# Performance work log

Measured on AMD Instinct MI355X. Metric: run time of the kernel, lower is better.

The kernel has to match this reference:

```python
import jax, jax.numpy as jnp
import numpy as np
from jax import lax

DIM = 384
D_STATE = 16
EXPAND = 2
D_INNER = DIM * EXPAND
B, H, W = 8, 32, 32


def setup_inputs() -> dict:
    key = jax.random.key(0)
    ks = jax.random.split(key, 16)
    s = 0.02
    return {
        'x': jax.random.normal(ks[0], (B, H, W, DIM), jnp.float32),
        'ln_g': jnp.ones((DIM,), jnp.float32),
        'ln_b': jnp.zeros((DIM,), jnp.float32),
        'mlp_w1': jax.random.normal(ks[1], (4, 32), jnp.float32) * s,
        'mlp_b1': jnp.zeros((32,), jnp.float32),
        'mlp_w2': jax.random.normal(ks[2], (32, 4), jnp.float32) * s,
        'mlp_b2': jnp.zeros((4,), jnp.float32),
        'in_proj_w': jax.random.normal(ks[3], (DIM, 2 * D_INNER), jnp.float32) * s,
        'conv_w': jax.random.normal(ks[4], (D_INNER, 1, 3), jnp.float32) * s,
        'conv_b': jnp.zeros((D_INNER,), jnp.float32),
        'x_proj_w': jax.random.normal(ks[5], (D_INNER, 2 * D_STATE), jnp.float32) * s,
        'dt_w': jax.random.normal(ks[6], (D_INNER, D_INNER), jnp.float32) * s,
        'dt_b': jnp.zeros((D_INNER,), jnp.float32),
        'A_log': jax.random.normal(ks[7], (D_INNER, D_STATE), jnp.float32) * 0.01,
        'D': jnp.ones((D_INNER,), jnp.float32),
        'out_proj_w': jax.random.normal(ks[8], (D_INNER, DIM), jnp.float32) * s,
    }


def _select_direction(xn, mlp_w1, mlp_b1, mlp_w2, mlp_b2):
    # GradientDirectionSelector (topk=1 -> argmax)
    b, h, w, _ = xn.shape
    xg = xn.mean(-1)[:, None]                                   # [B,1,H,W]
    xp = jnp.pad(xg, ((0, 0), (0, 0), (1, 1), (1, 1)), mode='reflect')
    kh = jnp.array([-1.0, 0.0, 1.0], xn.dtype).reshape(1, 1, 1, 3)
    kv = jnp.array([-1.0, 0.0, 1.0], xn.dtype).reshape(1, 1, 3, 1)
    dn = ('NCHW', 'OIHW', 'NCHW')
    gh = jnp.abs(lax.conv_general_dilated(xp, kh, (1, 1), 'VALID', dimension_numbers=dn))  # [B,1,H+2,W]
    gv = jnp.abs(lax.conv_general_dilated(xp, kv, (1, 1), 'VALID', dimension_numbers=dn))  # [B,1,H,W+2]
    gh = jax.image.resize(gh, (b, 1, h, w), 'bilinear')
    gv = jax.image.resize(gv, (b, 1, h, w), 'bilinear')
    gd = (gh + gv) * 0.5
    ga = jnp.abs(gh - gv)

    def pool_mean(g):  # avg_pool2d(3, stride=1, pad=1, count_include_pad=True), then spatial mean
        p = lax.reduce_window(g, 0.0, lax.add, (1, 1, 3, 3), (1, 1, 1, 1),
                              [(0, 0), (0, 0), (1, 1), (1, 1)]) / 9.0
        return p.mean(axis=(2, 3))  # [B,1]

    scores = jnp.concatenate([pool_mean(gh), pool_mean(gv), pool_mean(gd), pool_mean(ga)], axis=1)
    logits = jax.nn.relu(scores @ mlp_w1 + mlp_b1) @ mlp_w2 + mlp_b2
    return jnp.argmax(logits, axis=-1)  # softmax is monotone; topk(1) == argmax


def _ssm(seq, in_proj_w, conv_w, conv_b, x_proj_w, dt_w, dt_b, A_log, D, out_proj_w):
    b, L, _ = seq.shape
    xz = seq @ in_proj_w
    xc, z = xz[..., :D_INNER], xz[..., D_INNER:]
    xcc = jnp.swapaxes(xc, 1, 2)  # [B,Di,L]
    xcc = lax.conv_general_dilated(xcc, conv_w, (1,), [(1, 1)],
                                   feature_group_count=D_INNER,
                                   dimension_numbers=('NCH', 'OIH', 'NCH')) + conv_b[None, :, None]
    xc = jax.nn.silu(jnp.swapaxes(xcc, 1, 2))  # [B,L,Di]
    BC = xc @ x_proj_w
    Bm, Cm = BC[..., :D_STATE], BC[..., D_STATE:]
    delta = jax.nn.softplus(xc @ dt_w + dt_b)
    A = -jnp.exp(A_log)
    dA = jnp.exp(jnp.einsum('bld,dn->bldn', delta, A))        # [B,L,Di,N]
    dBx = (delta * xc)[..., None] * Bm[:, :, None, :]          # [B,L,Di,N]

    def step(hst, inp):
        dA_t, dBx_t, C_t = inp
        hst = dA_t * hst + dBx_t
        return hst, jnp.einsum('bdn,bn->bd', hst, C_t)

    h0 = jnp.zeros((b, D_INNER, D_STATE), xc.dtype)
    _, ys = lax.scan(step, h0, (jnp.swapaxes(dA, 0, 1), jnp.swapaxes(dBx, 0, 1), jnp.swapaxes(Cm, 0, 1)))
    y = jnp.swapaxes(ys, 0, 1) + D * xc
    y = y * jax.nn.silu(z)
    return y @ out_proj_w


def reference(x, ln_g, ln_b, mlp_w1, mlp_b1, mlp_w2, mlp_b2,
              in_proj_w, conv_w, conv_b, x_proj_w, dt_w, dt_b, A_log, D, out_proj_w):
    b, h, w, c = x.shape
    mu = x.mean(-1, keepdims=True)
    var = jnp.mean((x - mu) ** 2, axis=-1, keepdims=True)
    xn = (x - mu) / jnp.sqrt(var + 1e-5) * ln_g + ln_b

    idx = _select_direction(xn, mlp_w1, mlp_b1, mlp_w2, mlp_b2)  # [B]
    # DIRECTIONS_4: only 'vertical' (idx 1) changes scan order (transpose H/W);
    # diag directions alias horizontal in the source. Unscan is always (h w).
    is_vert = (idx % 4 == 1)[:, None, None, None]
    x_in = jnp.where(is_vert, jnp.swapaxes(xn, 1, 2), xn)  # requires H == W
    seq = x_in.reshape(b, h * w, c)
    out = _ssm(seq, in_proj_w, conv_w, conv_b, x_proj_w, dt_w, dt_b, A_log, D, out_proj_w)
    return x + out.reshape(b, h, w, c)
```

## Files before the change

kernel.cpp:

```cpp
#include <hip/hip_runtime.h>
#include <hip/hip_bf16.h>
#include <math.h>

#define NPOS 8192
#define DIMC 384
#define DIN 768
#define DST 16
#define CHUNK 16
#define NCH 64

typedef unsigned int uint;
typedef __attribute__((ext_vector_type(8))) short bf16x8;
typedef __attribute__((ext_vector_type(4))) float f32x4;

__device__ __forceinline__ float b2f(unsigned short u) {
    return __uint_as_float(((unsigned int)u) << 16);
}
__device__ __forceinline__ uint cvt_pk(float lo, float hi) {
    uint r;
    asm("v_cvt_pk_bf16_f32 %0, %1, %2" : "=v"(r) : "v"(lo), "v"(hi));
    return r;
}
__device__ __forceinline__ unsigned short f2b1(float f) {
    return (unsigned short)cvt_pk(f, f);
}
__device__ __forceinline__ float frcp(float x) {
    float r;
    asm("v_rcp_f32 %0, %1" : "=v"(r) : "v"(x));
    return r;
}
__device__ __forceinline__ float fexp2(float x) {
    float r;
    asm("v_exp_f32 %0, %1" : "=v"(r) : "v"(x));
    return r;
}
__device__ __forceinline__ void ub8(uint4 u, float* o) {
    o[0] = b2f((unsigned short)(u.x & 0xffff));
    o[1] = b2f((unsigned short)(u.x >> 16));
    o[2] = b2f((unsigned short)(u.y & 0xffff));
    o[3] = b2f((unsigned short)(u.y >> 16));
    o[4] = b2f((unsigned short)(u.z & 0xffff));
    o[5] = b2f((unsigned short)(u.z >> 16));
    o[6] = b2f((unsigned short)(u.w & 0xffff));
    o[7] = b2f((unsigned short)(u.w >> 16));
}
__device__ __forceinline__ void ld_bf8(const unsigned short* p, float* o) {
    ub8(*(const uint4*)p, o);
}
__device__ __forceinline__ uint4 pack_bf8(const float* o) {
    uint4 p;
    p.x = cvt_pk(o[0], o[1]);
    p.y = cvt_pk(o[2], o[3]);
    p.z = cvt_pk(o[4], o[5]);
    p.w = cvt_pk(o[6], o[7]);
    return p;
}
#define LOG2E 1.442695040888963f

__global__ __launch_bounds__(256) void k_ln(const float* __restrict__ x,
        const float* __restrict__ g, const float* __restrict__ bta,
        unsigned short* __restrict__ xnb, float* __restrict__ xg) {
    int wid = blockIdx.x * 4 + (threadIdx.x >> 6);
    int lane = threadIdx.x & 63;
    const float* xr = x + (size_t)wid * DIMC;
    float v[6];
    float s = 0.f, ss = 0.f;
#pragma unroll
    for (int i = 0; i < 6; i++) {
        v[i] = xr[lane + i * 64];
        s += v[i]; ss += v[i] * v[i];
    }
#pragma unroll
    for (int m = 32; m; m >>= 1) { s += __shfl_xor(s, m); ss += __shfl_xor(ss, m); }
    float mu = s * (1.f / DIMC);
    float var = ss * (1.f / DIMC) - mu * mu;
    float rstd = rsqrtf(var + 1e-5f);
    unsigned short* xnr = xnb + (size_t)wid * DIMC;
    float sn = 0.f;
#pragma unroll
    for (int i = 0; i < 6; i++) {
        int c = lane + i * 64;
        float o = (v[i] - mu) * rstd * g[c] + bta[c];
        xnr[c] = f2b1(o);
        sn += o;
    }
#pragma unroll
    for (int m = 32; m; m >>= 1) sn += __shfl_xor(sn, m);
    if (lane == 0) xg[wid] = sn * (1.f / DIMC);
}

__global__ __launch_bounds__(256) void k_dir(const float* __restrict__ xg,
        const float* __restrict__ w1, const float* __restrict__ b1,
        const float* __restrict__ w2, const float* __restrict__ b2,
        int* __restrict__ vert) {
    __shared__ float sg[32][32];
    __shared__ float red[4][4];
    int b = blockIdx.x;
    int tid = threadIdx.x;
    for (int i = tid; i < 1024; i += 256) sg[i >> 5][i & 31] = xg[b * 1024 + i];
    __syncthreads();
    float ph = 0, pv = 0, pd = 0, pa = 0;
    const float iks = 1.f / 1.0625f;
    for (int p = tid; p < 1024; p += 256) {
        int y = p >> 5, xq = p & 31;
        int xl = (xq >= 1) ? xq - 1 : 1;
        int xr2 = (xq <= 30) ? xq + 1 : 30;
        float sf = (y + 0.5f) * 1.0625f - 0.5f;
        int jlo = (int)ceilf(sf - 1.0625f); if (jlo < 0) jlo = 0;
        int jhi = (int)floorf(sf + 1.0625f); if (jhi > 33) jhi = 33;
        float acc = 0.f, wsum = 0.f;
        for (int j = jlo; j <= jhi; j++) {
            float wgt = 1.f - fabsf(sf - j) * iks;
            if (wgt <= 0.f) continue;
            int ry = (j >= 1) ? ((j <= 32) ? j - 1 : 30) : 1;
            acc += wgt * fabsf(sg[ry][xr2] - sg[ry][xl]);
            wsum += wgt;
        }
        float ghr = acc / wsum;
        int yu = (y >= 1) ? y - 1 : 1;
        int yd = (y <= 30) ? y + 1 : 30;
        float sfx = (xq + 0.5f) * 1.0625f - 0.5f;
        int ilo = (int)ceilf(sfx - 1.0625f); if (ilo < 0) ilo = 0;
        int ihi = (int)floorf(sfx + 1.0625f); if (ihi > 33) ihi = 33;
        float accv = 0.f, wsv = 0.f;
        for (int i = ilo; i <= ihi; i++) {
            float wgt = 1.f - fabsf(sfx - i) * iks;
            if (wgt <= 0.f) continue;
            int rx = (i >= 1) ? ((i <= 32) ? i - 1 : 30) : 1;
            accv += wgt * fabsf(sg[yd][rx] - sg[yu][rx]);
            wsv += wgt;
        }
        float gvr = accv / wsv;
        float gd = (ghr + gvr) * 0.5f;
        float ga = fabsf(ghr - gvr);
        float cw = ((y == 0 || y == 31) ? 2.f : 3.f) * ((xq == 0 || xq == 31) ? 2.f : 3.f);
        ph += ghr * cw; pv += gvr * cw; pd += gd * cw; pa += ga * cw;
    }
#pragma unroll
    for (int m = 32; m; m >>= 1) {
        ph += __shfl_xor(ph, m); pv += __shfl_xor(pv, m);
        pd += __shfl_xor(pd, m); pa += __shfl_xor(pa, m);
    }
    int wv = tid >> 6;
    if ((tid & 63) == 0) { red[wv][0] = ph; red[wv][1] = pv; red[wv][2] = pd; red[wv][3] = pa; }
    __syncthreads();
    if (tid == 0) {
        float sc[4];
        for (int k = 0; k < 4; k++)
            sc[k] = (red[0][k] + red[1][k] + red[2][k] + red[3][k]) * (1.f / 9216.f);
        float hdn[32];
        for (int j = 0; j < 32; j++) {
            float a = b1[j];
            for (int i = 0; i < 4; i++) a += sc[i] * w1[i * 32 + j];
            hdn[j] = a > 0.f ? a : 0.f;
        }
        float best = -1e30f; int bi = 0;
        for (int k = 0; k < 4; k++) {
            float a = b2[k];
            for (int j = 0; j < 32; j++) a += hdn[j] * w2[j * 4 + k];
            if (a > best) { best = a; bi = k; }
        }
        vert[b] = (bi == 1) ? 1 : 0;
    }
}

__device__ __forceinline__ void wt_body(const float* __restrict__ W,
        unsigned short* __restrict__ WT, int K, int N, int bid, int tid,
        float (*t)[33]) {
    int nb = N >> 5;
    int n0 = (bid % nb) << 5, k0 = (bid / nb) << 5;
    int kr = tid >> 3, n4 = (tid & 7) << 2;
    float4 v = *(const float4*)(W + (size_t)(k0 + kr) * N + n0 + n4);
    t[kr][n4 + 0] = v.x; t[kr][n4 + 1] = v.y; t[kr][n4 + 2] = v.z; t[kr][n4 + 3] = v.w;
    __syncthreads();
    int nr = tid >> 3, k4 = (tid & 7) << 2;
    ushort4 o;
    o.x = f2b1(t[k4 + 0][nr]); o.y = f2b1(t[k4 + 1][nr]);
    o.z = f2b1(t[k4 + 2][nr]); o.w = f2b1(t[k4 + 3][nr]);
    *(ushort4*)(WT + (size_t)(n0 + nr) * K + k0 + k4) = o;
}

__global__ __launch_bounds__(256) void k_prep(const float* __restrict__ inw,
        const float* __restrict__ dtw, const float* __restrict__ xpw,
        const float* __restrict__ outw,
        unsigned short* __restrict__ inwT, unsigned short* __restrict__ dtwTp,
        unsigned short* __restrict__ outwT) {
    __shared__ float t[32][33];
    int bid = blockIdx.x;
    int tid = threadIdx.x;
    if (bid < 576) {
        wt_body(inw, inwT, 384, 1536, bid, tid, t);
    } else if (bid < 1152) {
        wt_body(dtw, dtwTp, 768, 768, bid - 576, tid, t);
    } else if (bid < 1176) {
        wt_body(xpw, dtwTp + 768 * 768, 768, 32, bid - 1152, tid, t);
    } else if (bid < 1464) {
        wt_body(outw, outwT, 768, 384, bid - 1176, tid, t);
    } else {
        int i = (bid - 1464) * 256 + tid;
        if (i < (96 * 768) / 4)
            *(ushort4*)(dtwTp + 800 * 768 + i * 4) = (ushort4){0, 0, 0, 0};
    }
}

template <int MODE>
__global__ __launch_bounds__(256) void k_mfma(
        const unsigned short* __restrict__ op1,
        const unsigned short* __restrict__ op2,
        void* __restrict__ outp,
        const float* __restrict__ bias,
        const float* __restrict__ resid,
        const int* __restrict__ vert) {
    constexpr int K = (MODE == 0) ? 384 : 768;
    constexpr int NK = K / 32;
    constexpr int NBN = (MODE == 0) ? 12 : (MODE == 1 ? 7 : 3);
    __shared__ unsigned short lds[2][2][128 * 40];
    int tid = threadIdx.x;
    int bid = blockIdx.x;
    int xcd = bid & 7;
    int ii = bid >> 3;
    int n0 = (ii % NBN) << 7;
    int m0 = ((xcd << 3) + ii / NBN) << 7;
    int drow = tid >> 1, dkh = (tid & 1) << 4;

    size_t g1row, g2row;
    if constexpr (MODE == 0) {
        g1row = (size_t)(n0 + drow) * 384;
        int m = m0 + drow;
        int b = m >> 10, l = m & 1023;
        int src = vert[b] ? (((l & 31) << 5) | (l >> 5)) : l;
        g2row = ((size_t)(b << 10) + src) * 384;
    } else if constexpr (MODE == 1) {
        g1row = (size_t)(n0 + drow) * 768;
        g2row = (size_t)(m0 + drow) * 768;
    } else {
        g1row = (size_t)(m0 + drow) * 768;
        g2row = (size_t)(n0 + drow) * 768;
    }

    f32x4 acc[4][4];
    f32x4 zero = {0.f, 0.f, 0.f, 0.f};
#pragma unroll
    for (int i = 0; i < 4; i++)
#pragma unroll
        for (int j = 0; j < 4; j++) acc[i][j] = zero;

    uint4 s1a, s1b, s2a, s2b;
#define LOADS(k0_)                                              \
    { const unsigned short* p1 = op1 + g1row + (k0_) + dkh;     \
      s1a = *(const uint4*)p1; s1b = *(const uint4*)(p1 + 8);   \
      const unsigned short* p2 = op2 + g2row + (k0_) + dkh;     \
      s2a = *(const uint4*)p2; s2b = *(const uint4*)(p2 + 8); }
#define WRITES(buf_)                                            \
    { *(uint4*)&lds[buf_][0][drow * 40 + dkh] = s1a;            \
      *(uint4*)&lds[buf_][0][drow * 40 + dkh + 8] = s1b;        \
      *(uint4*)&lds[buf_][1][drow * 40 + dkh] = s2a;            \
      *(uint4*)&lds[buf_][1][drow * 40 + dkh + 8] = s2b; }

    int wid = tid >> 6, lane = tid & 63;
    int lr = lane & 15, lg = lane >> 4;
    int o1b = (wid >> 1) << 6;
    int o2b = (wid & 1) << 6;

    LOADS(0)
    WRITES(0)
    int cur = 0;
    for (int ks = 0; ks < NK; ks++) {
        int kn = (ks + 1) << 5;
        if (ks + 1 < NK) { LOADS(kn) }
        __syncthreads();
        const unsigned short* L1 = &lds[cur][0][0];
        const unsigned short* L2 = &lds[cur][1][0];
        bf16x8 f1[4], f2[4];
#pragma unroll
        for (int f = 0; f < 4; f++) f1[f] = *(const bf16x8*)&L1[(o1b + f * 16 + lr) * 40 + (lg << 3)];
#pragma unroll
        for (int f = 0; f < 4; f++) f2[f] = *(const bf16x8*)&L2[(o2b + f * 16 + lr) * 40 + (lg << 3)];
#pragma unroll
        for (int i = 0; i < 4; i++)
#pragma unroll
            for (int j = 0; j < 4; j++)
                acc[i][j] = __builtin_amdgcn_mfma_f32_16x16x32_bf16(f1[i], f2[j], acc[i][j], 0, 0, 0);
        if (ks + 1 < NK) { WRITES(cur ^ 1) }
        cur ^= 1;
    }

    if constexpr (MODE <= 1) {
        if (MODE == 1 && n0 == 768) {
            if ((wid >> 1) == 0) {
                float* BCT_ = (float*)resid;
#pragma unroll
                for (int i = 0; i < 2; i++) {
                    int col = i * 16 + lg * 4;
#pragma unroll
                    for (int j = 0; j < 4; j++) {
                        int mb_ = m0 + o2b + j * 16 + lr;
                        float4 v4;
                        v4.x = acc[i][j][0]; v4.y = acc[i][j][1];
                        v4.z = acc[i][j][2]; v4.w = acc[i][j][3];
                        *(float4*)(BCT_ + (size_t)mb_ * 32 + col) = v4;
                    }
                }
            }
        } else {
            __syncthreads();
            unsigned short* lt = &lds[0][0][0];
#pragma unroll
            for (int i = 0; i < 4; i++) {
                int nr = o1b + i * 16 + lg * 4;
#pragma unroll
                for (int j = 0; j < 4; j++) {
                    int mc = o2b + j * 16 + lr;
#pragma unroll
                    for (int r = 0; r < 4; r++) {
                        float v = acc[i][j][r];
                        if constexpr (MODE == 1) {
                            v += bias[n0 + nr + r];
                            v = fmaxf(v, 0.f) + __logf(1.f + __expf(-fabsf(v)));
                        }
                        lt[(nr + r) * 132 + mc] = f2b1(v);
                    }
                }
            }
            __syncthreads();
            unsigned short* CT = (unsigned short*)outp;
#pragma unroll
            for (int ps = 0; ps < 8; ps++) {
                int row = ps * 16 + (tid >> 4);
                uint4 v = *(const uint4*)&lt[row * 132 + (tid & 15) * 8];
                *(uint4*)(CT + (size_t)(n0 + row) * 8192 + m0 + (tid & 15) * 8) = v;
            }
        }
    } else {
        float* C = (float*)outp;
#pragma unroll
        for (int i = 0; i < 4; i++) {
            int mb_ = m0 + o1b + i * 16 + lg * 4;
#pragma unroll
            for (int j = 0; j < 4; j++) {
                int n = n0 + o2b + j * 16 + lr;
#pragma unroll
                for (int r = 0; r < 4; r++) {
                    int m = mb_ + r;
                    C[(size_t)m * 384 + n] = acc[i][j][r] + resid[(size_t)m * 384 + n];
                }
            }
        }
    }
#undef LOADS
#undef WRITES
}

__global__ __launch_bounds__(256) void k_conv(const unsigned short* __restrict__ xzb,
        const float* __restrict__ cw, const float* __restrict__ cb,
        unsigned short* __restrict__ xcT, unsigned short* __restrict__ xcR) {
    __shared__ unsigned short ly[128][64];
    int blk = blockIdx.x;
    int dg = blk % 12, mg = blk / 12;
    int r0 = mg * 128;
    int tid = threadIdx.x;
    int dl = tid >> 2, tq = tid & 3;
    int d = dg * 64 + dl;
    int t0 = r0 + tq * 32;
    const unsigned short* xr = xzb + (size_t)d * 8192;
    float xx[32];
#pragma unroll
    for (int q = 0; q < 4; q++) ub8(*(const uint4*)(xr + t0 + q * 8), xx + q * 8);
    int l0 = t0 & 1023;
    float xprev = (l0 != 0)   ? b2f(xr[t0 - 1])  : 0.f;
    float xnext = (l0 != 992) ? b2f(xr[t0 + 32]) : 0.f;
    float w0 = cw[d * 3], w1 = cw[d * 3 + 1], w2 = cw[d * 3 + 2], bb = cb[d];
    float o[32];
#pragma unroll
    for (int j = 0; j < 32; j++) {
        float v = bb + w1 * xx[j];
        v += w0 * ((j == 0) ? xprev : xx[j - 1]);
        v += w2 * ((j == 31) ? xnext : xx[j + 1]);
        o[j] = v * frcp(1.f + __expf(-v));
    }
    unsigned short* dstT = xcT + (size_t)d * 8192 + t0;
#pragma unroll
    for (int q = 0; q < 4; q++) *(uint4*)(dstT + q * 8) = pack_bf8(o + q * 8);
#pragma unroll
    for (int j = 0; j < 32; j++) ly[tq * 32 + j][dl] = f2b1(o[j]);
    __syncthreads();
#pragma unroll
    for (int k = 0; k < 4; k++) {
        int i = tid + k * 256;
        int row = i >> 3, sg = i & 7;
        uint4 v = *(const uint4*)&ly[row][sg * 8];
        *(uint4*)(xcR + (size_t)(r0 + row) * 768 + dg * 64 + sg * 8) = v;
    }
}

__global__ __launch_bounds__(256) void k_scan1(const unsigned short* __restrict__ xzb,
        const unsigned short* __restrict__ xcT, const float* __restrict__ BCT,
        const float* __restrict__ A_log,
        unsigned short* __restrict__ G, float* __restrict__ sumd) {
    int tid = threadIdx.x;
    int lane = tid & 63;
    int blk = blockIdx.x;
    int dg = blk % 12;
    int cg = (blk / 12) % 16;
    int b  = blk / 192;
    int c = cg * 4 + (tid >> 6);
    int d = dg * 64 + lane;
    int r0i = __builtin_amdgcn_readfirstlane(b * 1024 + c * CHUNK);
    const float* Bu = BCT + (size_t)r0i * 32;
    float Avl[16];
#pragma unroll
    for (int q = 0; q < 4; q++) {
        float4 a4 = *(const float4*)(A_log + d * 16 + q * 4);
        Avl[q * 4 + 0] = -__expf(a4.x) * LOG2E;
        Avl[q * 4 + 1] = -__expf(a4.y) * LOG2E;
        Avl[q * 4 + 2] = -__expf(a4.z) * LOG2E;
        Avl[q * 4 + 3] = -__expf(a4.w) * LOG2E;
    }
    const unsigned short* dptr = xzb + (size_t)d * 8192 + r0i;
    const unsigned short* xptr = xcT + (size_t)d * 8192 + r0i;
    uint4 du[2], xu[2];
#pragma unroll
    for (int q = 0; q < 2; q++) {
        du[q] = *(const uint4*)(dptr + q * 8);
        xu[q] = *(const uint4*)(xptr + q * 8);
    }
    float h[16] = {};
    float sd = 0.f;
#pragma unroll
    for (int q = 0; q < 2; q++) {
        float dv[8], xv[8];
        ub8(du[q], dv);
        ub8(xu[q], xv);
#pragma unroll
        for (int j = 0; j < 8; j++) {
            int t = q * 8 + j;
            float dx = dv[j] * xv[j];
            sd += dv[j];
            float Bt[16];
            *(float4*)&Bt[0]  = *(const float4*)(Bu + t * 32);
            *(float4*)&Bt[4]  = *(const float4*)(Bu + t * 32 + 4);
            *(float4*)&Bt[8]  = *(const float4*)(Bu + t * 32 + 8);
            *(float4*)&Bt[12] = *(const float4*)(Bu + t * 32 + 12);
#pragma unroll
            for (int n = 0; n < 16; n++)
                h[n] = fmaf(fexp2(dv[j] * Avl[n]), h[n], dx * Bt[n]);
        }
    }
    unsigned short* gp = G + (((size_t)(b * NCH + c)) * 768 + d) * 16;
    *(uint4*)gp       = pack_bf8(h);
    *(uint4*)(gp + 8) = pack_bf8(h + 8);
    sumd[(size_t)(b * NCH + c) * 768 + d] = sd;
}

__global__ __launch_bounds__(256) void k_scan2(unsigned short* __restrict__ G,
        const float* __restrict__ sumd, const float* __restrict__ A_log) {
    int blk = blockIdx.x;
    int dg = blk % 48, b = blk / 48;
    int tid = threadIdx.x;
    int dl = tid >> 4, n = tid & 15;
    int d = dg * 16 + dl;
    float Av = -__expf(A_log[d * 16 + n]);
    float H = 0.f;
#pragma unroll 8
    for (int c = 0; c < NCH; c++) {
        size_t gi = (((size_t)(b * NCH + c)) * 768 + d) * 16 + n;
        float Gv = b2f(G[gi]);
        float P = __expf(Av * sumd[(size_t)(b * NCH + c) * 768 + d]);
        G[gi] = f2b1(H);
        H = fmaf(P, H, Gv);
    }
}

__global__ __launch_bounds__(256) void k_scan3(const unsigned short* __restrict__ xzb,
        const unsigned short* __restrict__ xcT, const float* __restrict__ BCT,
        const float* __restrict__ A_log, const float* __restrict__ Dp,
        const unsigned short* __restrict__ G, unsigned short* __restrict__ yR) {
    __shared__ unsigned short ly[64][64];
    int tid = threadIdx.x;
    int lane = tid & 63;
    int wv = tid >> 6;
    int blk = blockIdx.x;
    int dg = blk % 12;
    int cg = (blk / 12) % 16;
    int b  = blk / 192;
    int c = cg * 4 + wv;
    int d = dg * 64 + lane;
    int r0i = __builtin_amdgcn_readfirstlane(b * 1024 + c * CHUNK);
    const float* Bu = BCT + (size_t)r0i * 32;
    float Avl[16];
#pragma unroll
    for (int q = 0; q < 4; q++) {
        float4 a4 = *(const float4*)(A_log + d * 16 + q * 4);
        Avl[q * 4 + 0] = -__expf(a4.x) * LOG2E;
        Avl[q * 4 + 1] = -__expf(a4.y) * LOG2E;
        Avl[q * 4 + 2] = -__expf(a4.z) * LOG2E;
        Avl[q * 4 + 3] = -__expf(a4.w) * LOG2E;
    }
    float Dv = Dp[d];
    const unsigned short* dptr = xzb + (size_t)d * 8192 + r0i;
    const unsigned short* zptr = xzb + (size_t)(768 + d) * 8192 + r0i;
    const unsigned short* xptr = xcT + (size_t)d * 8192 + r0i;
    uint4 du[2], xu[2], zu[2];
#pragma unroll
    for (int q = 0; q < 2; q++) {
        du[q] = *(const uint4*)(dptr + q * 8);
        xu[q] = *(const uint4*)(xptr + q * 8);
        zu[q] = *(const uint4*)(zptr + q * 8);
    }
    float h[16];
    {
        const unsigned short* gp = G + (((size_t)(b * NCH + c)) * 768 + d) * 16;
        ld_bf8(gp, h);
        ld_bf8(gp + 8, h + 8);
    }
#pragma unroll
    for (int q = 0; q < 2; q++) {
        float dv[8], xv[8], zv[8];
        ub8(du[q], dv);
        ub8(xu[q], xv);
        ub8(zu[q], zv);
#pragma unroll
        for (int j = 0; j < 8; j++) {
            int t = q * 8 + j;
            float dx = dv[j] * xv[j];
            float Bt[16], Ct[16];
            *(float4*)&Bt[0]  = *(const float4*)(Bu + t * 32);
            *(float4*)&Bt[4]  = *(const float4*)(Bu + t * 32 + 4);
            *(float4*)&Bt[8]  = *(const float4*)(Bu + t * 32 + 8);
            *(float4*)&Bt[12] = *(const float4*)(Bu + t * 32 + 12);
            *(float4*)&Ct[0]  = *(const float4*)(Bu + t * 32 + 16);
            *(float4*)&Ct[4]  = *(const float4*)(Bu + t * 32 + 20);
            *(float4*)&Ct[8]  = *(const float4*)(Bu + t * 32 + 24);
            *(float4*)&Ct[12] = *(const float4*)(Bu + t * 32 + 28);
            float p0 = 0.f, p1 = 0.f, p2 = 0.f, p3 = 0.f;
#pragma unroll
            for (int n = 0; n < 16; n += 4) {
                h[n + 0] = fmaf(fexp2(dv[j] * Avl[n + 0]), h[n + 0], dx * Bt[n + 0]);
                h[n + 1] = fmaf(fexp2(dv[j] * Avl[n + 1]), h[n + 1], dx * Bt[n + 1]);
                h[n + 2] = fmaf(fexp2(dv[j] * Avl[n + 2]), h[n + 2], dx * Bt[n + 2]);
                h[n + 3] = fmaf(fexp2(dv[j] * Avl[n + 3]), h[n + 3], dx * Bt[n + 3]);
                p0 = fmaf(h[n + 0], Ct[n + 0], p0);
                p1 = fmaf(h[n + 1], Ct[n + 1], p1);
                p2 = fmaf(h[n + 2], Ct[n + 2], p2);
                p3 = fmaf(h[n + 3], Ct[n + 3], p3);
            }
            float p = (p0 + p1) + (p2 + p3);
            float zz = zv[j];
            float sig = frcp(1.f + __expf(-zz));
            ly[wv * 16 + t][lane] = f2b1(fmaf(Dv, xv[j], p) * zz * sig);
        }
    }
    __syncthreads();
    size_t rb = (size_t)b * 1024 + (size_t)cg * 64;
#pragma unroll
    for (int k = 0; k < 2; k++) {
        int i = tid + k * 256;
        int row = i >> 3, sg = i & 7;
        uint4 v = *(const uint4*)&ly[row][sg * 8];
        *(uint4*)(yR + (size_t)(rb + row) * 768 + dg * 64 + sg * 8) = v;
    }
}

extern "C" void kernel_launch(void* const* d_in, const int* in_sizes, int n_in,
                              void* d_out, int out_size, void* d_ws, size_t ws_size,
                              hipStream_t stream) {
    const float* x    = (const float*)d_in[0];
    const float* ln_g = (const float*)d_in[1];
    const float* ln_b = (const float*)d_in[2];
    const float* mw1  = (const float*)d_in[3];
    const float* mb1  = (const float*)d_in[4];
    const float* mw2  = (const float*)d_in[5];
    const float* mb2  = (const float*)d_in[6];
    const float* inw  = (const float*)d_in[7];
    const float* cw   = (const float*)d_in[8];
    const float* cb   = (const float*)d_in[9];
    const float* xpw  = (const float*)d_in[10];
    const float* dtw  = (const float*)d_in[11];
    const float* dtb  = (const float*)d_in[12];
    const float* alog = (const float*)d_in[13];
    const float* Dp   = (const float*)d_in[14];
    const float* outw = (const float*)d_in[15];
    float* out = (float*)d_out;

    char* ws = (char*)d_ws;
    unsigned short* xzb = (unsigned short*)(ws);
    float* BCT = (float*)(ws + 25165824);
    float* xg  = (float*)(ws + 26214400);
    int*  vert = (int*)(ws + 26247168);
    unsigned short* G = (unsigned short*)(ws + 26248192);
    float* sumd = (float*)(ws + 38831104);
    unsigned short* inwT  = (unsigned short*)(ws + 40403968);
    unsigned short* dtwTp = (unsigned short*)(ws + 41583616);
    unsigned short* outwT = (unsigned short*)(ws + 42959872);
    unsigned short* xcR   = (unsigned short*)(ws + 43549696);
    unsigned short* yR    = (unsigned short*)(ws + 56132608);

    unsigned short* xnb = (unsigned short*)d_out;
    unsigned short* xcT = (unsigned short*)d_out;

    k_ln<<<2048, 256, 0, stream>>>(x, ln_g, ln_b, xnb, xg);
    k_dir<<<8, 256, 0, stream>>>(xg, mw1, mb1, mw2, mb2, vert);
    k_prep<<<1536, 256, 0, stream>>>(inw, dtw, xpw, outw, inwT, dtwTp, outwT);
    k_mfma<0><<<12 * 64, 256, 0, stream>>>(inwT, xnb, xzb, nullptr, nullptr, vert);
    k_conv<<<12 * 64, 256, 0, stream>>>(xzb, cw, cb, xcT, xcR);
    k_mfma<1><<<7 * 64, 256, 0, stream>>>(dtwTp, xcR, xzb, dtb, (const float*)BCT, nullptr);
    k_scan1<<<1536, 256, 0, stream>>>(xzb, xcT, BCT, alog, G, sumd);
    k_scan2<<<8 * 48, 256, 0, stream>>>(G, sumd, alog);
    k_scan3<<<1536, 256, 0, stream>>>(xzb, xcT, BCT, alog, Dp, G, yR);
    k_mfma<2><<<3 * 64, 256, 0, stream>>>(yR, outwT, out, nullptr, x, nullptr);
}
```

Baseline: 153.3 us.

## Use 64x128 GEMM tiles with 192-wide K phases loaded in bulk into LDS

```diff
diff --git a/kernel.cpp b/kernel.cpp
--- a/kernel.cpp
+++ b/kernel.cpp
@@ -211,90 +211,104 @@
         const float* __restrict__ bias,
         const float* __restrict__ resid,
         const int* __restrict__ vert) {
-    constexpr int K = (MODE == 0) ? 384 : 768;
-    constexpr int NK = K / 32;
-    constexpr int NBN = (MODE == 0) ? 12 : (MODE == 1 ? 7 : 3);
-    __shared__ unsigned short lds[2][2][128 * 40];
+    constexpr int ldK = (MODE == 0) ? 384 : 768;
+    constexpr int NPH = (MODE == 0) ? 2 : 4;
+    __shared__ unsigned short s1[64 * 200];
+    __shared__ unsigned short s2[128 * 200];
     int tid = threadIdx.x;
     int bid = blockIdx.x;
     int xcd = bid & 7;
     int ii = bid >> 3;
-    int n0 = (ii % NBN) << 7;
-    int m0 = ((xcd << 3) + ii / NBN) << 7;
-    int drow = tid >> 1, dkh = (tid & 1) << 4;
-
-    size_t g1row, g2row;
-    if constexpr (MODE == 0) {
-        g1row = (size_t)(n0 + drow) * 384;
-        int m = m0 + drow;
-        int b = m >> 10, l = m & 1023;
-        int src = vert[b] ? (((l & 31) << 5) | (l >> 5)) : l;
-        g2row = ((size_t)(b << 10) + src) * 384;
-    } else if constexpr (MODE == 1) {
-        g1row = (size_t)(n0 + drow) * 768;
-        g2row = (size_t)(m0 + drow) * 768;
-    } else {
-        g1row = (size_t)(m0 + drow) * 768;
-        g2row = (size_t)(n0 + drow) * 768;
-    }
-
-    f32x4 acc[4][4];
+    int p1, p2;
+    if constexpr (MODE == 0)      { p1 = (ii % 24) << 6; p2 = ((xcd << 3) + ii / 24) << 7; }
+    else if constexpr (MODE == 1) { p1 = (ii % 14) << 6; p2 = ((xcd << 3) + ii / 14) << 7; }
+    else                          { p2 = (ii % 3) << 7;  p1 = ((xcd << 4) + ii / 3) << 6; }
+
+    int vt = 0;
+    if constexpr (MODE == 0) vt = vert[p2 >> 10];
+
+    f32x4 acc[2][4];
     f32x4 zero = {0.f, 0.f, 0.f, 0.f};
 #pragma unroll
-    for (int i = 0; i < 4; i++)
+    for (int i = 0; i < 2; i++)
 #pragma unroll
         for (int j = 0; j < 4; j++) acc[i][j] = zero;
 
-    uint4 s1a, s1b, s2a, s2b;
-#define LOADS(k0_)                                              \
-    { const unsigned short* p1 = op1 + g1row + (k0_) + dkh;     \
-      s1a = *(const uint4*)p1; s1b = *(const uint4*)(p1 + 8);   \
-      const unsigned short* p2 = op2 + g2row + (k0_) + dkh;     \
-      s2a = *(const uint4*)p2; s2b = *(const uint4*)(p2 + 8); }
-#define WRITES(buf_)                                            \
-    { *(uint4*)&lds[buf_][0][drow * 40 + dkh] = s1a;            \
-      *(uint4*)&lds[buf_][0][drow * 40 + dkh + 8] = s1b;        \
-      *(uint4*)&lds[buf_][1][drow * 40 + dkh] = s2a;            \
-      *(uint4*)&lds[buf_][1][drow * 40 + dkh + 8] = s2b; }
-
-    int wid = tid >> 6, lane = tid & 63;
+    int w = tid >> 6, lane = tid & 63;
     int lr = lane & 15, lg = lane >> 4;
-    int o1b = (wid >> 1) << 6;
-    int o2b = (wid & 1) << 6;
-
-    LOADS(0)
-    WRITES(0)
-    int cur = 0;
-    for (int ks = 0; ks < NK; ks++) {
-        int kn = (ks + 1) << 5;
-        if (ks + 1 < NK) { LOADS(kn) }
+    int o1b = (w & 1) << 5;
+    int o2b = (w >> 1) << 6;
+
+    for (int ph = 0; ph < NPH; ph++) {
+        if (ph) __syncthreads();
+        int kc = ph * 192;
+        {
+            uint4 v[6];
+#pragma unroll
+            for (int q = 0; q < 6; q++) {
+                int u = tid + q * 256;
+                int r = u / 24, cb = (u % 24) << 3;
+                v[q] = *(const uint4*)(op1 + (size_t)(p1 + r) * ldK + kc + cb);
+            }
+#pragma unroll
+            for (int q = 0; q < 6; q++) {
+                int u = tid + q * 256;
+                int r = u / 24, cb = (u % 24) << 3;
+                *(uint4*)&s1[r * 200 + cb] = v[q];
+            }
+        }
+#pragma unroll
+        for (int g = 0; g < 2; g++) {
+            uint4 v[6];
+#pragma unroll
+            for (int q = 0; q < 6; q++) {
+                int u = tid + (g * 6 + q) * 256;
+                int r = u / 24, cb = (u % 24) << 3;
+                size_t grow;
+                if constexpr (MODE == 0) {
+                    int m = p2 + r;
+                    int l = m & 1023;
+                    int src = vt ? (((l & 31) << 5) | (l >> 5)) : l;
+                    grow = (size_t)((m & ~1023) + src) * 384;
+                } else {
+                    grow = (size_t)(p2 + r) * 768;
+                }
+                v[q] = *(const uint4*)(op2 + grow + kc + cb);
+            }
+#pragma unroll
+            for (int q = 0; q < 6; q++) {
+                int u = tid + (g * 6 + q) * 256;
+                int r = u / 24, cb = (u % 24) << 3;
+                *(uint4*)&s2[r * 200 + cb] = v[q];
+            }
+        }
         __syncthreads();
-        const unsigned short* L1 = &lds[cur][0][0];
-        const unsigned short* L2 = &lds[cur][1][0];
-        bf16x8 f1[4], f2[4];
-#pragma unroll
-        for (int f = 0; f < 4; f++) f1[f] = *(const bf16x8*)&L1[(o1b + f * 16 + lr) * 40 + (lg << 3)];
-#pragma unroll
-        for (int f = 0; f < 4; f++) f2[f] = *(const bf16x8*)&L2[(o2b + f * 16 + lr) * 40 + (lg << 3)];
-#pragma unroll
-        for (int i = 0; i < 4; i++)
-#pragma unroll
-            for (int j = 0; j < 4; j++)
-                acc[i][j] = __builtin_amdgcn_mfma_f32_16x16x32_bf16(f1[i], f2[j], acc[i][j], 0, 0, 0);
-        if (ks + 1 < NK) { WRITES(cur ^ 1) }
-        cur ^= 1;
+#pragma unroll
+        for (int st = 0; st < 6; st++) {
+            int col = st * 32 + (lg << 3);
+            bf16x8 f1[2], f2[4];
+#pragma unroll
+            for (int f = 0; f < 2; f++) f1[f] = *(const bf16x8*)&s1[(o1b + f * 16 + lr) * 200 + col];
+#pragma unroll
+            for (int f = 0; f < 4; f++) f2[f] = *(const bf16x8*)&s2[(o2b + f * 16 + lr) * 200 + col];
+#pragma unroll
+            for (int i = 0; i < 2; i++)
+#pragma unroll
+                for (int j = 0; j < 4; j++)
+                    acc[i][j] = __builtin_amdgcn_mfma_f32_16x16x32_bf16(f1[i], f2[j], acc[i][j], 0, 0, 0);
+        }
     }
 
     if constexpr (MODE <= 1) {
-        if (MODE == 1 && n0 == 768) {
-            if ((wid >> 1) == 0) {
+        if (MODE == 1 && p1 >= 768) {
+            if (p1 == 768 && (w & 1) == 0) {
                 float* BCT_ = (float*)resid;
 #pragma unroll
                 for (int i = 0; i < 2; i++) {
                     int col = i * 16 + lg * 4;
 #pragma unroll
                     for (int j = 0; j < 4; j++) {
-                        int mb_ = m0 + o2b + j * 16 + lr;
+                        int mb_ = p2 + o2b + j * 16 + lr;
                         float4 v4;
                         v4.x = acc[i][j][0]; v4.y = acc[i][j][1];
                         v4.z = acc[i][j][2]; v4.w = acc[i][j][3];
@@ -304,9 +318,9 @@
             }
         } else {
             __syncthreads();
-            unsigned short* lt = &lds[0][0][0];
-#pragma unroll
-            for (int i = 0; i < 4; i++) {
+            unsigned short* lt = s2;
+#pragma unroll
+            for (int i = 0; i < 2; i++) {
                 int nr = o1b + i * 16 + lg * 4;
 #pragma unroll
                 for (int j = 0; j < 4; j++) {
@@ -315,7 +329,7 @@
                     for (int r = 0; r < 4; r++) {
                         float v = acc[i][j][r];
                         if constexpr (MODE == 1) {
-                            v += bias[n0 + nr + r];
+                            v += bias[p1 + nr + r];
                             v = fmaxf(v, 0.f) + __logf(1.f + __expf(-fabsf(v)));
                         }
                         lt[(nr + r) * 132 + mc] = f2b1(v);
@@ -325,20 +339,20 @@
             __syncthreads();
             unsigned short* CT = (unsigned short*)outp;
 #pragma unroll
-            for (int ps = 0; ps < 8; ps++) {
+            for (int ps = 0; ps < 4; ps++) {
                 int row = ps * 16 + (tid >> 4);
                 uint4 v = *(const uint4*)&lt[row * 132 + (tid & 15) * 8];
-                *(uint4*)(CT + (size_t)(n0 + row) * 8192 + m0 + (tid & 15) * 8) = v;
+                *(uint4*)(CT + (size_t)(p1 + row) * 8192 + p2 + (tid & 15) * 8) = v;
             }
         }
     } else {
         float* C = (float*)outp;
 #pragma unroll
-        for (int i = 0; i < 4; i++) {
-            int mb_ = m0 + o1b + i * 16 + lg * 4;
+        for (int i = 0; i < 2; i++) {
+            int mb_ = p1 + o1b + i * 16 + lg * 4;
 #pragma unroll
             for (int j = 0; j < 4; j++) {
-                int n = n0 + o2b + j * 16 + lr;
+                int n = p2 + o2b + j * 16 + lr;
 #pragma unroll
                 for (int r = 0; r < 4; r++) {
                     int m = mb_ + r;
@@ -347,8 +361,6 @@
             }
         }
     }
-#undef LOADS
-#undef WRITES
 }
 
 __global__ __launch_bounds__(256) void k_conv(const unsigned short* __restrict__ xzb,
@@ -601,11 +613,11 @@
     k_ln<<<2048, 256, 0, stream>>>(x, ln_g, ln_b, xnb, xg);
     k_dir<<<8, 256, 0, stream>>>(xg, mw1, mb1, mw2, mb2, vert);
     k_prep<<<1536, 256, 0, stream>>>(inw, dtw, xpw, outw, inwT, dtwTp, outwT);
-    k_mfma<0><<<12 * 64, 256, 0, stream>>>(inwT, xnb, xzb, nullptr, nullptr, vert);
+    k_mfma<0><<<24 * 64, 256, 0, stream>>>(inwT, xnb, xzb, nullptr, nullptr, vert);
     k_conv<<<12 * 64, 256, 0, stream>>>(xzb, cw, cb, xcT, xcR);
-    k_mfma<1><<<7 * 64, 256, 0, stream>>>(dtwTp, xcR, xzb, dtb, (const float*)BCT, nullptr);
+    k_mfma<1><<<14 * 64, 256, 0, stream>>>(dtwTp, xcR, xzb, dtb, (const float*)BCT, nullptr);
     k_scan1<<<1536, 256, 0, stream>>>(xzb, xcT, BCT, alog, G, sumd);
     k_scan2<<<8 * 48, 256, 0, stream>>>(G, sumd, alog);
     k_scan3<<<1536, 256, 0, stream>>>(xzb, xcT, BCT, alog, Dp, G, yR);
-    k_mfma<2><<<3 * 64, 256, 0, stream>>>(yR, outwT, out, nullptr, x, nullptr);
-}
+    k_mfma<2><<<128 * 3, 256, 0, stream>>>(yR, outwT, out, nullptr, x, nullptr);
+}
```

After: 158.4 us. 3.3% more time.
